# Kernel tuning notes

Measured on AMD Instinct MI355X. Metric: run time of the kernel, lower is better.

The kernel has to match this reference:

```python
import jax, jax.numpy as jnp
import numpy as np

B = 256          # graphs per batch
NC, NP = 16384, 131072   # compound / protein node counts
EC, EP = 131072, 2097152 # edge counts
D = 128


def _gconv(x, src, dst, W, b, n):
    # DGL GraphConv, norm='both': h = D_in^{-1/2} A D_out^{-1/2} x W + b
    ones = jnp.ones(src.shape, x.dtype)
    out_deg = jax.ops.segment_sum(ones, src, num_segments=n)
    in_deg = jax.ops.segment_sum(ones, dst, num_segments=n)
    ns = jax.lax.rsqrt(jnp.maximum(out_deg, 1.0))
    nd = jax.lax.rsqrt(jnp.maximum(in_deg, 1.0))
    h = (x * ns[:, None]) @ W           # apply weight before aggregation (same math, less traffic)
    m = jax.ops.segment_sum(h[src], dst, num_segments=n)  # SpMM aggregation
    return m * nd[:, None] + b


def _mean_nodes(x, gid, nb):
    s = jax.ops.segment_sum(x, gid, num_segments=nb)
    cnt = jax.ops.segment_sum(jnp.ones((x.shape[0],), x.dtype), gid, num_segments=nb)
    return s / jnp.maximum(cnt, 1.0)[:, None]


def setup_inputs() -> dict:
    key = jax.random.key(0)
    ks = jax.random.split(key, 24)
    s = 0.05
    inp = {
        "compound_feat": jax.random.normal(ks[0], (NC, 74), jnp.float32),
        "protein_feat": jax.random.normal(ks[1], (NP, 128), jnp.float32),
        # graph structure
        "c_src": jax.random.randint(ks[2], (EC,), 0, NC, jnp.int32),
        "c_dst": jax.random.randint(ks[3], (EC,), 0, NC, jnp.int32),
        "p_src": jax.random.randint(ks[4], (EP,), 0, NP, jnp.int32),
        "p_dst": jax.random.randint(ks[5], (EP,), 0, NP, jnp.int32),
        "c_gid": jax.random.randint(ks[6], (NC,), 0, B, jnp.int32),
        "p_gid": jax.random.randint(ks[7], (NP,), 0, B, jnp.int32),
        # GraphConv params
        "Wc1": jax.random.normal(ks[8], (74, D), jnp.float32) * s,
        "bc1": jnp.zeros((D,), jnp.float32),
        "Wc2": jax.random.normal(ks[9], (D, D), jnp.float32) * s,
        "bc2": jnp.zeros((D,), jnp.float32),
        "Wp1": jax.random.normal(ks[10], (128, D), jnp.float32) * s,
        "bp1": jnp.zeros((D,), jnp.float32),
        "Wp2": jax.random.normal(ks[11], (D, D), jnp.float32) * s,
        "bp2": jnp.zeros((D,), jnp.float32),
        # predictor MLP
        "Wf1": jax.random.normal(ks[12], (2 * D, D), jnp.float32) * s,
        "bf1": jnp.zeros((D,), jnp.float32),
        "Wf2": jax.random.normal(ks[13], (D, 1), jnp.float32) * s,
        "bf2": jnp.zeros((1,), jnp.float32),
    }
    return inp


def reference(compound_feat, protein_feat, c_src, c_dst, p_src, p_dst, c_gid, p_gid,
              Wc1, bc1, Wc2, bc2, Wp1, bp1, Wp2, bp2, Wf1, bf1, Wf2, bf2):
    c = jax.nn.relu(_gconv(compound_feat, c_src, c_dst, Wc1, bc1, NC))
    c = jax.nn.relu(_gconv(c, c_src, c_dst, Wc2, bc2, NC))
    c_global = _mean_nodes(c, c_gid, B)                     # [B, D]
    p = jax.nn.relu(_gconv(protein_feat, p_src, p_dst, Wp1, bp1, NP))
    p = jax.nn.relu(_gconv(p, p_src, p_dst, Wp2, bp2, NP))
    p_global = _mean_nodes(p, p_gid, B)                     # [B, D]
    combined = jnp.concatenate([c_global, p_global], axis=1)  # [B, 2D]
    h = jax.nn.relu(combined @ Wf1 + bf1)
    out = h @ Wf2 + bf2                                     # [B, 1]
    return out.squeeze(-1)
```

## Files before the change

kernel.cpp:

```cpp
#include <hip/hip_runtime.h>
#include <hip/hip_fp16.h>

#define D 128
#define SCH 4096
#define NBLK 256

typedef _Float16 half8 __attribute__((ext_vector_type(8)));
typedef float f32x4 __attribute__((ext_vector_type(4)));

struct HTask { const int* keys; int n; int shift; int* H; };
struct H6 { HTask t[6]; };

struct SPTask { const int* in; int n; int* part; };
struct SP6 { SPTask t[6]; };

struct SDTask { const int* in; int n; const int* part; int* out; int* total; };
struct SD6 { SDTask t[6]; };

struct ScTask { const int* k1; const int* k2; int n; int shift;
                const int* base1; const int* base2;
                int* o1; int* o2k; int* o2v; int mode; };
struct Sc4 { ScTask t[4]; };

struct CTask { const int* tmpk; const int* base; int n; int fine; int* deg; };
struct C4 { CTask t[4]; };

struct NTask { const int* outdeg; const int* indeg; float* ns; float* nd; int n; };
struct N2 { NTask t[2]; };

struct LTask { const int* tmpk; const int* tmpv; const int* base; int n;
               const int* rowptr; int shift; int fine; int* col; };
struct L2T { LTask t[2]; };

struct WPk { const float* W; _Float16* out; int K; };
struct W4 { WPk t[4]; };

struct GTask { const float* x; const float* ns; const _Float16* Wp; __half* h; int K; };
struct GemP { GTask t[2]; int nb0; };

struct ATask { const __half* h; const int* rowptr; const int* col;
               const float* nd; const float* b; void* out; int halfOut; };
struct AggP { ATask t[2]; int np; int ntot; };

struct MTask { const __half* x; const int* gbase; int n; const int* list; float* out; };
struct M2 { MTask t[2]; };


__global__ __launch_bounds__(256) void k_hist_all(H6 P) {
  HTask tk = P.t[blockIdx.y];
  __shared__ int bins[256];
  int blk = blockIdx.x, t = threadIdx.x;
  bins[t] = 0;
  __syncthreads();
  int per = (tk.n + NBLK - 1) / NBLK;
  int beg = blk * per, end = min(beg + per, tk.n);
  for (int i = beg + t; i < end; i += 256)
    atomicAdd(&bins[tk.keys[i] >> tk.shift], 1);
  __syncthreads();
  tk.H[t * NBLK + blk] = bins[t];
}

__global__ __launch_bounds__(256) void k_scan_part_all(SP6 P) {
  SPTask tk = P.t[blockIdx.y];
  int b = blockIdx.x, t = threadIdx.x;
  int base = b * SCH;
  int s = 0;
  for (int i = t; i < SCH; i += 256) {
    int idx = base + i;
    if (idx < tk.n) s += tk.in[idx];
  }
  __shared__ int red[256];
  red[t] = s;
  __syncthreads();
  for (int d = 128; d > 0; d >>= 1) {
    if (t < d) red[t] += red[t + d];
    __syncthreads();
  }
  if (t == 0) tk.part[b] = red[0];
}

__global__ __launch_bounds__(256) void k_scan_down_all(SD6 P) {
  SDTask tk = P.t[blockIdx.y];
  int b = blockIdx.x, t = threadIdx.x;
  int lane = t & 63, wid = t >> 6;
  __shared__ int wsum[4];
  if (b == 0 && t == 0 && tk.total) {
    int s = 0;
    for (int w = 0; w < (int)gridDim.x; ++w) s += tk.part[w];
    *tk.total = s;
  }
  int offset = 0;
  for (int w = 0; w < b; ++w) offset += tk.part[w];
  int base = b * SCH;
  if (base >= tk.n) return;
  int idx0 = base + t * 16;
  int v[16];
  int s = 0;
#pragma unroll
  for (int i = 0; i < 16; ++i) {
    int idx = idx0 + i;
    v[i] = (idx < tk.n) ? tk.in[idx] : 0;
    s += v[i];
  }
  int inc = s;
  for (int d = 1; d < 64; d <<= 1) {
    int u = __shfl_up(inc, d, 64);
    if (lane >= d) inc += u;
  }
  if (lane == 63) wsum[wid] = inc;
  __syncthreads();
  int woff = 0;
  for (int w = 0; w < wid; ++w) woff += wsum[w];
  int ex = offset + woff + inc - s;
#pragma unroll
  for (int i = 0; i < 16; ++i) {
    int idx = idx0 + i;
    if (idx < tk.n) tk.out[idx] = ex;
    ex += v[i];
  }
}

__global__ __launch_bounds__(256) void k_scatter_all(Sc4 P) {
  ScTask tk = P.t[blockIdx.y];
  __shared__ int curA[256], curB[256];
  int blk = blockIdx.x, t = threadIdx.x;
  curA[t] = tk.base1[t * NBLK + blk];
  if (tk.mode == 0) curB[t] = tk.base2[t * NBLK + blk];
  __syncthreads();
  int per = (tk.n + NBLK - 1) / NBLK;
  int beg = blk * per, end = min(beg + per, tk.n);
  if (tk.mode == 0) {
    for (int i = beg + t; i < end; i += 256) {
      int s = tk.k1[i], d = tk.k2[i];
      int pa = atomicAdd(&curA[s >> tk.shift], 1);
      tk.o1[pa] = s;
      int pb = atomicAdd(&curB[d >> tk.shift], 1);
      tk.o2k[pb] = d;
      tk.o2v[pb] = s;
    }
  } else {
    for (int i = beg + t; i < end; i += 256) {
      int pa = atomicAdd(&curA[tk.k1[i] >> tk.shift], 1);
      tk.o1[pa] = i;
    }
  }
}

__global__ __launch_bounds__(256) void k_l2count_all(C4 P) {
  CTask tk = P.t[blockIdx.y];
  __shared__ int bins[512];
  int b = blockIdx.x, t = threadIdx.x;
  for (int f = t; f < tk.fine; f += 256) bins[f] = 0;
  __syncthreads();
  int beg = tk.base[b * NBLK];
  int end = (b == NBLK - 1) ? tk.n : tk.base[(b + 1) * NBLK];
  for (int i = beg + t; i < end; i += 256)
    atomicAdd(&bins[tk.tmpk[i] & (tk.fine - 1)], 1);
  __syncthreads();
  for (int f = t; f < tk.fine; f += 256)
    tk.deg[b * tk.fine + f] = bins[f];
}

__global__ __launch_bounds__(256) void k_norms_all(N2 P) {
  NTask tk = P.t[blockIdx.y];
  int i = blockIdx.x * blockDim.x + threadIdx.x;
  if (i < tk.n) {
    tk.ns[i] = rsqrtf(fmaxf((float)tk.outdeg[i], 1.f));
    tk.nd[i] = rsqrtf(fmaxf((float)tk.indeg[i], 1.f));
  }
}

__global__ __launch_bounds__(256) void k_l2scatter_all(L2T P) {
  LTask tk = P.t[blockIdx.y];
  __shared__ int cur[512];
  int b = blockIdx.x, t = threadIdx.x;
  int v0 = b << tk.shift;
  for (int f = t; f < tk.fine; f += 256) cur[f] = tk.rowptr[v0 + f];
  __syncthreads();
  int beg = tk.base[b * NBLK];
  int end = (b == NBLK - 1) ? tk.n : tk.base[(b + 1) * NBLK];
  for (int i = beg + t; i < end; i += 256) {
    int pos = atomicAdd(&cur[tk.tmpk[i] & (tk.fine - 1)], 1);
    tk.col[pos] = tk.tmpv[i];
  }
}


__global__ __launch_bounds__(256) void k_wpack(W4 P) {
  WPk tk = P.t[blockIdx.y];
  int f = blockIdx.x;
  int kch = (tk.K + 31) >> 5;
  if (f >= (kch << 3)) return;
  int kc = f >> 3, nt = f & 7;
  int t = threadIdx.x;
  int l = t & 63, e0 = (t >> 6) << 1;
  int col = (nt << 4) + (l & 15);
  int kb = (kc << 5) + ((l >> 4) << 3);
#pragma unroll
  for (int e = e0; e < e0 + 2; ++e) {
    int k = kb + e;
    float v = (k < tk.K) ? tk.W[(size_t)k * D + col] : 0.f;
    tk.out[(((size_t)f * 64 + l) << 3) + e] = (_Float16)v;
  }
}

__global__ __launch_bounds__(256) void k_nl_gemm(GemP P) {
  __shared__ __align__(16) _Float16 Bs[32 * 64 * 8];
  int bx = blockIdx.x;
  GTask tk;
  int v0;
  if (bx < P.nb0) { tk = P.t[0]; v0 = bx * 128; }
  else            { tk = P.t[1]; v0 = (bx - P.nb0) * 128; }
  const int K = tk.K;
  const int kch = (K + 31) >> 5;
  int t = threadIdx.x, w = t >> 6, l = t & 63;

  {
    const uint4* src = (const uint4*)tk.Wp;
    uint4* dst = (uint4*)Bs;
    int n16 = kch << 9;
    for (int i = t; i < n16; i += 256) dst[i] = src[i];
  }
  __syncthreads();

  int row = l & 15;
  int ks = (l >> 4) << 3;
  int m0 = v0 + (w << 5);
  const float* x0 = tk.x + (size_t)(m0 + row) * K + ks;
  const float* x1 = tk.x + (size_t)(m0 + 16 + row) * K + ks;

  f32x4 acc[2][8];
  f32x4 zero = {0.f, 0.f, 0.f, 0.f};
#pragma unroll
  for (int i = 0; i < 2; ++i)
#pragma unroll
    for (int j = 0; j < 8; ++j) acc[i][j] = zero;

  for (int kc = 0; kc < kch; ++kc) {
    half8 a0, a1;
    if (K == D) {
      float4 p0 = *(const float4*)(x0 + (kc << 5));
      float4 p1 = *(const float4*)(x0 + (kc << 5) + 4);
      float4 q0 = *(const float4*)(x1 + (kc << 5));
      float4 q1 = *(const float4*)(x1 + (kc << 5) + 4);
      a0[0] = (_Float16)p0.x; a0[1] = (_Float16)p0.y;
      a0[2] = (_Float16)p0.z; a0[3] = (_Float16)p0.w;
      a0[4] = (_Float16)p1.x; a0[5] = (_Float16)p1.y;
      a0[6] = (_Float16)p1.z; a0[7] = (_Float16)p1.w;
      a1[0] = (_Float16)q0.x; a1[1] = (_Float16)q0.y;
      a1[2] = (_Float16)q0.z; a1[3] = (_Float16)q0.w;
      a1[4] = (_Float16)q1.x; a1[5] = (_Float16)q1.y;
      a1[6] = (_Float16)q1.z; a1[7] = (_Float16)q1.w;
    } else {
#pragma unroll
      for (int e = 0; e < 8; ++e) {
        int k = (kc << 5) + ks + e;
        a0[e] = (k < K) ? (_Float16)x0[(kc << 5) + e] : (_Float16)0.f;
        a1[e] = (k < K) ? (_Float16)x1[(kc << 5) + e] : (_Float16)0.f;
      }
    }
#pragma unroll
    for (int nt = 0; nt < 8; ++nt) {
      half8 b = *(const half8*)&Bs[(size_t)((((kc << 3) + nt) << 6) + l) << 3];
      acc[0][nt] = __builtin_amdgcn_mfma_f32_16x16x32_f16(a0, b, acc[0][nt], 0, 0, 0);
      acc[1][nt] = __builtin_amdgcn_mfma_f32_16x16x32_f16(a1, b, acc[1][nt], 0, 0, 0);
    }
  }

  int rr = (l >> 4) << 2;
  int c0 = l & 15;
#pragma unroll
  for (int mt = 0; mt < 2; ++mt) {
    int vb = m0 + (mt << 4) + rr;
    float s0 = tk.ns[vb], s1 = tk.ns[vb + 1];
    float s2 = tk.ns[vb + 2], s3 = tk.ns[vb + 3];
#pragma unroll
    for (int nt = 0; nt < 8; ++nt) {
      __half* hp = tk.h + (size_t)vb * D + (nt << 4) + c0;
      hp[0]     = __float2half_rn(acc[mt][nt][0] * s0);
      hp[D]     = __float2half_rn(acc[mt][nt][1] * s1);
      hp[2 * D] = __float2half_rn(acc[mt][nt][2] * s2);
      hp[3 * D] = __float2half_rn(acc[mt][nt][3] * s3);
    }
  }
}

__global__ __launch_bounds__(256) void k_aggregate(AggP P) {
  int wid = threadIdx.x >> 6;
  int lane = threadIdx.x & 63;
  int gv = blockIdx.x * 4 + wid;
  if (gv >= P.ntot) return;
  ATask tk;
  int v;
  if (gv < P.np) { tk = P.t[0]; v = gv; }
  else           { tk = P.t[1]; v = gv - P.np; }
  int beg = tk.rowptr[v], end = tk.rowptr[v + 1];
  int f0 = (lane & 15) * 8;
  int rsel = lane >> 4;
  const __half* h = tk.h;
  const int* col = tk.col;

  float acc[8];
#pragma unroll
  for (int k = 0; k < 8; ++k) acc[k] = 0.f;

  for (int j = beg; j < end; j += 8) {
    int j0 = j + rsel, j1 = j + 4 + rsel;
    if (j0 < end) {
      int c0 = col[j0];
      uint4 r = *(const uint4*)&h[(size_t)c0 * D + f0];
      const __half2* q = (const __half2*)&r;
#pragma unroll
      for (int k = 0; k < 4; ++k) {
        float2 f = __half22float2(q[k]);
        acc[2 * k] += f.x; acc[2 * k + 1] += f.y;
      }
    }
    if (j1 < end) {
      int c1 = col[j1];
      uint4 r = *(const uint4*)&h[(size_t)c1 * D + f0];
      const __half2* q = (const __half2*)&r;
#pragma unroll
      for (int k = 0; k < 4; ++k) {
        float2 f = __half22float2(q[k]);
        acc[2 * k] += f.x; acc[2 * k + 1] += f.y;
      }
    }
  }

#pragma unroll
  for (int k = 0; k < 8; ++k) {
    acc[k] += __shfl_down(acc[k], 32, 64);
    acc[k] += __shfl_down(acc[k], 16, 64);
  }

  if (rsel == 0) {
    float s = tk.nd[v];
    float4 b0 = *(const float4*)&tk.b[f0];
    float4 b1 = *(const float4*)&tk.b[f0 + 4];
    float r[8];
    r[0] = fmaxf(fmaf(acc[0], s, b0.x), 0.f);
    r[1] = fmaxf(fmaf(acc[1], s, b0.y), 0.f);
    r[2] = fmaxf(fmaf(acc[2], s, b0.z), 0.f);
    r[3] = fmaxf(fmaf(acc[3], s, b0.w), 0.f);
    r[4] = fmaxf(fmaf(acc[4], s, b1.x), 0.f);
    r[5] = fmaxf(fmaf(acc[5], s, b1.y), 0.f);
    r[6] = fmaxf(fmaf(acc[6], s, b1.z), 0.f);
    r[7] = fmaxf(fmaf(acc[7], s, b1.w), 0.f);
    if (tk.halfOut) {
      union { __half2 h2[4]; uint4 u; } pk;
#pragma unroll
      for (int k = 0; k < 4; ++k) {
        pk.h2[k].x = __float2half_rn(r[2 * k]);
        pk.h2[k].y = __float2half_rn(r[2 * k + 1]);
      }
      *(uint4*)&((__half*)tk.out)[(size_t)v * D + f0] = pk.u;
    } else {
      float4 o0 = {r[0], r[1], r[2], r[3]};
      float4 o1 = {r[4], r[5], r[6], r[7]};
      *(float4*)&((float*)tk.out)[(size_t)v * D + f0] = o0;
      *(float4*)&((float*)tk.out)[(size_t)v * D + f0 + 4] = o1;
    }
  }
}

__device__ __forceinline__ void acc_half4(float4& a, const __half* p) {
  uint2 r = *(const uint2*)p;
  __half2 q0 = *(__half2*)&r.x;
  __half2 q1 = *(__half2*)&r.y;
  float2 f0 = __half22float2(q0);
  float2 f1 = __half22float2(q1);
  a.x += f0.x; a.y += f0.y; a.z += f1.x; a.w += f1.y;
}

__global__ __launch_bounds__(256) void k_seg_mean(M2 P) {
  MTask tk = P.t[blockIdx.y];
  int g = blockIdx.x, t = threadIdx.x;
  int slot = t >> 5;
  int c = (t & 31) * 4;
  int beg = tk.gbase[g * NBLK];
  int end = (g == (int)gridDim.x - 1) ? tk.n : tk.gbase[(g + 1) * NBLK];
  const __half* x = tk.x;
  const int* list = tk.list;

  float4 a0 = make_float4(0.f, 0.f, 0.f, 0.f);
  float4 a1 = make_float4(0.f, 0.f, 0.f, 0.f);
  int j = beg + slot;
  for (; j + 8 < end; j += 16) {
    int s0 = list[j], s1 = list[j + 8];
    acc_half4(a0, x + (size_t)s0 * D + c);
    acc_half4(a1, x + (size_t)s1 * D + c);
  }
  if (j < end)
    acc_half4(a0, x + (size_t)list[j] * D + c);
  a0.x += a1.x; a0.y += a1.y; a0.z += a1.z; a0.w += a1.w;

  a0.x += __shfl_down(a0.x, 32, 64);
  a0.y += __shfl_down(a0.y, 32, 64);
  a0.z += __shfl_down(a0.z, 32, 64);
  a0.w += __shfl_down(a0.w, 32, 64);

  __shared__ float sred[4][32 * 4];
  int wid = t >> 6, lane = t & 63;
  if (lane < 32) *(float4*)&sred[wid][lane * 4] = a0;
  __syncthreads();
  if (t < 32) {
    float4 s0 = *(const float4*)&sred[0][t * 4];
    float4 s1 = *(const float4*)&sred[1][t * 4];
    float4 s2 = *(const float4*)&sred[2][t * 4];
    float4 s3 = *(const float4*)&sred[3][t * 4];
    float inv = 1.f / fmaxf((float)(end - beg), 1.f);
    float4 r;
    r.x = (s0.x + s1.x + s2.x + s3.x) * inv;
    r.y = (s0.y + s1.y + s2.y + s3.y) * inv;
    r.z = (s0.z + s1.z + s2.z + s3.z) * inv;
    r.w = (s0.w + s1.w + s2.w + s3.w) * inv;
    *(float4*)&tk.out[(size_t)g * D + c] = r;
  }
}

__global__ void k_mlp(const float* __restrict__ cg, const float* __restrict__ pg,
                      const float* __restrict__ Wf1, const float* __restrict__ bf1,
                      const float* __restrict__ Wf2, const float* __restrict__ bf2,
                      float* __restrict__ out) {
  __shared__ float xs[256];
  __shared__ float red[128];
  int b = blockIdx.x, t = threadIdx.x;
  xs[t] = cg[b * D + t];
  xs[128 + t] = pg[b * D + t];
  __syncthreads();
  float acc = bf1[t];
  for (int k = 0; k < 256; ++k) acc = fmaf(xs[k], Wf1[k * D + t], acc);
  float hv = fmaxf(acc, 0.f);
  red[t] = hv * Wf2[t];
  for (int d = 64; d > 0; d >>= 1) {
    __syncthreads();
    if (t < d) red[t] += red[t + d];
  }
  if (t == 0) out[b] = red[0] + bf2[0];
}


extern "C" void kernel_launch(void* const* d_in, const int* in_sizes, int n_in,
                              void* d_out, int out_size, void* d_ws, size_t ws_size,
                              hipStream_t stream) {
  const float* compound_feat = (const float*)d_in[0];
  const float* protein_feat  = (const float*)d_in[1];
  const int* c_src = (const int*)d_in[2];
  const int* c_dst = (const int*)d_in[3];
  const int* p_src = (const int*)d_in[4];
  const int* p_dst = (const int*)d_in[5];
  const int* c_gid = (const int*)d_in[6];
  const int* p_gid = (const int*)d_in[7];
  const float* Wc1 = (const float*)d_in[8];  const float* bc1 = (const float*)d_in[9];
  const float* Wc2 = (const float*)d_in[10]; const float* bc2 = (const float*)d_in[11];
  const float* Wp1 = (const float*)d_in[12]; const float* bp1 = (const float*)d_in[13];
  const float* Wp2 = (const float*)d_in[14]; const float* bp2 = (const float*)d_in[15];
  const float* Wf1 = (const float*)d_in[16]; const float* bf1 = (const float*)d_in[17];
  const float* Wf2 = (const float*)d_in[18]; const float* bf2 = (const float*)d_in[19];
  float* out = (float*)d_out;

  const int EC = in_sizes[2], EP = in_sizes[4];
  const int NC = in_sizes[6], NP = in_sizes[7];
  const int B  = out_size;
  const int KC = in_sizes[0] / NC;
  const int cshift = __builtin_ctz(NC / 256), cfine = NC / 256;
  const int pshift = __builtin_ctz(NP / 256), pfine = NP / 256;
  const int HN = 256 * NBLK;

  char* ws = (char*)d_ws;
  size_t off = 0;
  auto alloc = [&](size_t bytes) -> void* {
    void* p = ws + off;
    off += (bytes + 255) & ~(size_t)255;
    return p;
  };

  int* H0 = (int*)alloc((size_t)HN * 4);
  int* H1 = (int*)alloc((size_t)HN * 4);
  int* H2 = (int*)alloc((size_t)HN * 4);
  int* H3 = (int*)alloc((size_t)HN * 4);
  int* H4 = (int*)alloc((size_t)HN * 4);
  int* H5 = (int*)alloc((size_t)HN * 4);
  int* partH = (int*)alloc((size_t)6 * 32 * 4);
  int* partD = (int*)alloc((size_t)2 * 32 * 4);
  int* tmps_c = (int*)alloc((size_t)EC * 4);
  int* tmpd_c = (int*)alloc((size_t)EC * 4);
  int* tmpv_c = (int*)alloc((size_t)EC * 4);
  int* tmps_p = (int*)alloc((size_t)EP * 4);
  int* tmpd_p = (int*)alloc((size_t)EP * 4);
  int* tmpv_p = (int*)alloc((size_t)EP * 4);
  int* c_outdeg = (int*)alloc((size_t)NC * 4);
  int* c_indeg  = (int*)alloc((size_t)NC * 4);
  int* p_outdeg = (int*)alloc((size_t)NP * 4);
  int* p_indeg  = (int*)alloc((size_t)NP * 4);
  float* c_ns = (float*)alloc((size_t)NC * 4);
  float* c_nd = (float*)alloc((size_t)NC * 4);
  float* p_ns = (float*)alloc((size_t)NP * 4);
  float* p_nd = (float*)alloc((size_t)NP * 4);
  int* c_rowptr = (int*)alloc((size_t)(NC + 1) * 4);
  int* p_rowptr = (int*)alloc((size_t)(NP + 1) * 4);
  int* c_col   = (int*)alloc((size_t)EC * 4);
  int* p_col   = (int*)alloc((size_t)EP * 4);
  int* cg_list = (int*)alloc((size_t)NC * 4);
  int* pg_list = (int*)alloc((size_t)NP * 4);
  __half* c_h  = (__half*)alloc((size_t)NC * D * 2);
  float*  c_m1 = (float*) alloc((size_t)NC * D * 4);
  __half* c_m2 = (__half*)alloc((size_t)NC * D * 2);
  __half* p_h  = (__half*)alloc((size_t)NP * D * 2);
  float*  p_m1 = (float*) alloc((size_t)NP * D * 4);
  __half* p_m2 = (__half*)alloc((size_t)NP * D * 2);
  float* cg = (float*)alloc((size_t)B * D * 4);
  float* pg = (float*)alloc((size_t)B * D * 4);
  _Float16* wp_p1 = (_Float16*)alloc((size_t)32 * 1024);
  _Float16* wp_c1 = (_Float16*)alloc((size_t)32 * 1024);
  _Float16* wp_p2 = (_Float16*)alloc((size_t)32 * 1024);
  _Float16* wp_c2 = (_Float16*)alloc((size_t)32 * 1024);
  (void)ws_size; (void)n_in;

  {
    W4 PW = {{{Wp1, wp_p1, D}, {Wc1, wp_c1, KC}, {Wp2, wp_p2, D}, {Wc2, wp_c2, D}}};
    k_wpack<<<dim3(32, 4), 256, 0, stream>>>(PW);
  }
  {
    H6 P = {{{c_src, EC, cshift, H0}, {c_dst, EC, cshift, H1}, {c_gid, NC, 0, H2},
             {p_src, EP, pshift, H3}, {p_dst, EP, pshift, H4}, {p_gid, NP, 0, H5}}};
    k_hist_all<<<dim3(NBLK, 6), 256, 0, stream>>>(P);
  }
  {
    SP6 Pp = {{{H0, HN, partH + 0}, {H1, HN, partH + 32}, {H2, HN, partH + 64},
               {H3, HN, partH + 96}, {H4, HN, partH + 128}, {H5, HN, partH + 160}}};
    k_scan_part_all<<<dim3(16, 6), 256, 0, stream>>>(Pp);
    SD6 Pd = {{{H0, HN, partH + 0, H0, nullptr}, {H1, HN, partH + 32, H1, nullptr},
               {H2, HN, partH + 64, H2, nullptr}, {H3, HN, partH + 96, H3, nullptr},
               {H4, HN, partH + 128, H4, nullptr}, {H5, HN, partH + 160, H5, nullptr}}};
    k_scan_down_all<<<dim3(16, 6), 256, 0, stream>>>(Pd);
  }
  {
    Sc4 P = {{{c_src, c_dst, EC, cshift, H0, H1, tmps_c, tmpd_c, tmpv_c, 0},
              {p_src, p_dst, EP, pshift, H3, H4, tmps_p, tmpd_p, tmpv_p, 0},
              {c_gid, nullptr, NC, 0, H2, nullptr, cg_list, nullptr, nullptr, 1},
              {p_gid, nullptr, NP, 0, H5, nullptr, pg_list, nullptr, nullptr, 1}}};
    k_scatter_all<<<dim3(NBLK, 4), 256, 0, stream>>>(P);
  }
  {
    C4 P = {{{tmps_c, H0, EC, cfine, c_outdeg}, {tmpd_c, H1, EC, cfine, c_indeg},
             {tmps_p, H3, EP, pfine, p_outdeg}, {tmpd_p, H4, EP, pfine, p_indeg}}};
    k_l2count_all<<<dim3(NBLK, 4), 256, 0, stream>>>(P);
  }
  {
    SP6 Pp; Pp.t[0] = {c_indeg, NC, partD + 0}; Pp.t[1] = {p_indeg, NP, partD + 32};
    Pp.t[2] = Pp.t[3] = Pp.t[4] = Pp.t[5] = SPTask{c_indeg, 0, partD + 0};
    k_scan_part_all<<<dim3(32, 2), 256, 0, stream>>>(Pp);
    SD6 Pd; Pd.t[0] = {c_indeg, NC, partD + 0, c_rowptr, c_rowptr + NC};
    Pd.t[1] = {p_indeg, NP, partD + 32, p_rowptr, p_rowptr + NP};
    Pd.t[2] = Pd.t[3] = Pd.t[4] = Pd.t[5] = Pd.t[0];
    k_scan_down_all<<<dim3(32, 2), 256, 0, stream>>>(Pd);
  }
  {
    N2 P = {{{c_outdeg, c_indeg, c_ns, c_nd, NC}, {p_outdeg, p_indeg, p_ns, p_nd, NP}}};
    k_norms_all<<<dim3((NP + 255) / 256, 2), 256, 0, stream>>>(P);
  }
  {
    L2T P = {{{tmpd_c, tmpv_c, H1, EC, c_rowptr, cshift, cfine, c_col},
              {tmpd_p, tmpv_p, H4, EP, p_rowptr, pshift, pfine, p_col}}};
    k_l2scatter_all<<<dim3(NBLK, 2), 256, 0, stream>>>(P);
  }

  const int gnb = NP / 128 + NC / 128;
  const int anb = (NP + NC + 3) / 4;
  {
    GemP P = {{{protein_feat, p_ns, wp_p1, p_h, D}, {compound_feat, c_ns, wp_c1, c_h, KC}}, NP / 128};
    k_nl_gemm<<<gnb, 256, 0, stream>>>(P);
  }
  {
    AggP P = {{{p_h, p_rowptr, p_col, p_nd, bp1, p_m1, 0},
               {c_h, c_rowptr, c_col, c_nd, bc1, c_m1, 0}}, NP, NP + NC};
    k_aggregate<<<anb, 256, 0, stream>>>(P);
  }
  {
    GemP P = {{{p_m1, p_ns, wp_p2, p_h, D}, {c_m1, c_ns, wp_c2, c_h, D}}, NP / 128};
    k_nl_gemm<<<gnb, 256, 0, stream>>>(P);
  }
  {
    AggP P = {{{p_h, p_rowptr, p_col, p_nd, bp2, p_m2, 1},
               {c_h, c_rowptr, c_col, c_nd, bc2, c_m2, 1}}, NP, NP + NC};
    k_aggregate<<<anb, 256, 0, stream>>>(P);
  }
  {
    M2 P = {{{c_m2, H2, NC, cg_list, cg}, {p_m2, H5, NP, pg_list, pg}}};
    k_seg_mean<<<dim3(B, 2), 256, 0, stream>>>(P);
  }

  k_mlp<<<B, D, 0, stream>>>(cg, pg, Wf1, bf1, Wf2, bf2, out);
}
```

Baseline: 554.8 us.

## Drop src-side sort, count degrees atomically, store layer-1 output in fp16, deepen gather ILP

Removes the radix histogram, scatter and fine-count passes for source keys. Out- and in-degrees are now computed with global atomics over the raw edge arrays, which also eliminates the l2count kernel. The layer-1 aggregate output is stored as fp16 instead of fp32, and the second GEMM reads half8 directly, halving that intermediate traffic. The aggregation loop now issues four column loads before the gathers to increase memory-level parallelism. Global atomics on 2M edges may contend, and fp16 intermediates reduce precision.

```diff
diff --git a/kernel.cpp b/kernel.cpp
--- a/kernel.cpp
+++ b/kernel.cpp
@@ -17,13 +17,12 @@
 struct SDTask { const int* in; int n; const int* part; int* out; int* total; };
 struct SD6 { SDTask t[6]; };
 
+struct DgT { const int* keys; int n; int* deg; };
+struct Dg4 { DgT t[4]; };
+
 struct ScTask { const int* k1; const int* k2; int n; int shift;
-                const int* base1; const int* base2;
-                int* o1; int* o2k; int* o2v; int mode; };
+                const int* base; int* o1; int* o2; int mode; };
 struct Sc4 { ScTask t[4]; };
-
-struct CTask { const int* tmpk; const int* base; int n; int fine; int* deg; };
-struct C4 { CTask t[4]; };
 
 struct NTask { const int* outdeg; const int* indeg; float* ns; float* nd; int n; };
 struct N2 { NTask t[2]; };
@@ -35,7 +34,8 @@
 struct WPk { const float* W; _Float16* out; int K; };
 struct W4 { WPk t[4]; };
 
-struct GTask { const float* x; const float* ns; const _Float16* Wp; __half* h; int K; };
+struct GTask { const void* x; const float* ns; const _Float16* Wp; __half* h;
+               int K; int xh; };
 struct GemP { GTask t[2]; int nb0; };
 
 struct ATask { const __half* h; const int* rowptr; const int* col;
@@ -58,6 +58,13 @@
     atomicAdd(&bins[tk.keys[i] >> tk.shift], 1);
   __syncthreads();
   tk.H[t * NBLK + blk] = bins[t];
+}
+
+__global__ __launch_bounds__(256) void k_deg_all(Dg4 P) {
+  DgT tk = P.t[blockIdx.y];
+  int stride = gridDim.x * 256;
+  for (int i = blockIdx.x * 256 + threadIdx.x; i < tk.n; i += stride)
+    atomicAdd(&tk.deg[tk.keys[i]], 1);
 }
 
 __global__ __launch_bounds__(256) void k_scan_part_all(SP6 P) {
@@ -122,43 +129,25 @@
 
 __global__ __launch_bounds__(256) void k_scatter_all(Sc4 P) {
   ScTask tk = P.t[blockIdx.y];
-  __shared__ int curA[256], curB[256];
+  __shared__ int cur[256];
   int blk = blockIdx.x, t = threadIdx.x;
-  curA[t] = tk.base1[t * NBLK + blk];
-  if (tk.mode == 0) curB[t] = tk.base2[t * NBLK + blk];
+  cur[t] = tk.base[t * NBLK + blk];
   __syncthreads();
   int per = (tk.n + NBLK - 1) / NBLK;
   int beg = blk * per, end = min(beg + per, tk.n);
   if (tk.mode == 0) {
     for (int i = beg + t; i < end; i += 256) {
-      int s = tk.k1[i], d = tk.k2[i];
-      int pa = atomicAdd(&curA[s >> tk.shift], 1);
-      tk.o1[pa] = s;
-      int pb = atomicAdd(&curB[d >> tk.shift], 1);
-      tk.o2k[pb] = d;
-      tk.o2v[pb] = s;
+      int d = tk.k1[i], s = tk.k2[i];
+      int p = atomicAdd(&cur[d >> tk.shift], 1);
+      tk.o1[p] = d;
+      tk.o2[p] = s;
     }
   } else {
     for (int i = beg + t; i < end; i += 256) {
-      int pa = atomicAdd(&curA[tk.k1[i] >> tk.shift], 1);
-      tk.o1[pa] = i;
-    }
-  }
-}
-
-__global__ __launch_bounds__(256) void k_l2count_all(C4 P) {
-  CTask tk = P.t[blockIdx.y];
-  __shared__ int bins[512];
-  int b = blockIdx.x, t = threadIdx.x;
-  for (int f = t; f < tk.fine; f += 256) bins[f] = 0;
-  __syncthreads();
-  int beg = tk.base[b * NBLK];
-  int end = (b == NBLK - 1) ? tk.n : tk.base[(b + 1) * NBLK];
-  for (int i = beg + t; i < end; i += 256)
-    atomicAdd(&bins[tk.tmpk[i] & (tk.fine - 1)], 1);
-  __syncthreads();
-  for (int f = t; f < tk.fine; f += 256)
-    tk.deg[b * tk.fine + f] = bins[f];
+      int p = atomicAdd(&cur[tk.k1[i] >> tk.shift], 1);
+      tk.o1[p] = i;
+    }
+  }
 }
 
 __global__ __launch_bounds__(256) void k_norms_all(N2 P) {
@@ -226,8 +215,15 @@
   int row = l & 15;
   int ks = (l >> 4) << 3;
   int m0 = v0 + (w << 5);
-  const float* x0 = tk.x + (size_t)(m0 + row) * K + ks;
-  const float* x1 = tk.x + (size_t)(m0 + 16 + row) * K + ks;
+  const float* xf0 = nullptr; const float* xf1 = nullptr;
+  const _Float16* xh0 = nullptr; const _Float16* xh1 = nullptr;
+  if (tk.xh) {
+    xh0 = (const _Float16*)tk.x + (size_t)(m0 + row) * D + ks;
+    xh1 = xh0 + (size_t)16 * D;
+  } else {
+    xf0 = (const float*)tk.x + (size_t)(m0 + row) * K + ks;
+    xf1 = xf0 + (size_t)16 * K;
+  }
 
   f32x4 acc[2][8];
   f32x4 zero = {0.f, 0.f, 0.f, 0.f};
@@ -238,11 +234,14 @@
 
   for (int kc = 0; kc < kch; ++kc) {
     half8 a0, a1;
-    if (K == D) {
-      float4 p0 = *(const float4*)(x0 + (kc << 5));
-      float4 p1 = *(const float4*)(x0 + (kc << 5) + 4);
-      float4 q0 = *(const float4*)(x1 + (kc << 5));
-      float4 q1 = *(const float4*)(x1 + (kc << 5) + 4);
+    if (tk.xh) {
+      a0 = *(const half8*)(xh0 + (kc << 5));
+      a1 = *(const half8*)(xh1 + (kc << 5));
+    } else if (K == D) {
+      float4 p0 = *(const float4*)(xf0 + (kc << 5));
+      float4 p1 = *(const float4*)(xf0 + (kc << 5) + 4);
+      float4 q0 = *(const float4*)(xf1 + (kc << 5));
+      float4 q1 = *(const float4*)(xf1 + (kc << 5) + 4);
       a0[0] = (_Float16)p0.x; a0[1] = (_Float16)p0.y;
       a0[2] = (_Float16)p0.z; a0[3] = (_Float16)p0.w;
       a0[4] = (_Float16)p1.x; a0[5] = (_Float16)p1.y;
@@ -255,8 +254,8 @@
 #pragma unroll
       for (int e = 0; e < 8; ++e) {
         int k = (kc << 5) + ks + e;
-        a0[e] = (k < K) ? (_Float16)x0[(kc << 5) + e] : (_Float16)0.f;
-        a1[e] = (k < K) ? (_Float16)x1[(kc << 5) + e] : (_Float16)0.f;
+        a0[e] = (k < K) ? (_Float16)xf0[(kc << 5) + e] : (_Float16)0.f;
+        a1[e] = (k < K) ? (_Float16)xf1[(kc << 5) + e] : (_Float16)0.f;
       }
     }
 #pragma unroll
@@ -304,26 +303,24 @@
 #pragma unroll
   for (int k = 0; k < 8; ++k) acc[k] = 0.f;
 
-  for (int j = beg; j < end; j += 8) {
-    int j0 = j + rsel, j1 = j + 4 + rsel;
-    if (j0 < end) {
-      int c0 = col[j0];
-      uint4 r = *(const uint4*)&h[(size_t)c0 * D + f0];
-      const __half2* q = (const __half2*)&r;
-#pragma unroll
-      for (int k = 0; k < 4; ++k) {
-        float2 f = __half22float2(q[k]);
-        acc[2 * k] += f.x; acc[2 * k + 1] += f.y;
-      }
-    }
-    if (j1 < end) {
-      int c1 = col[j1];
-      uint4 r = *(const uint4*)&h[(size_t)c1 * D + f0];
-      const __half2* q = (const __half2*)&r;
-#pragma unroll
-      for (int k = 0; k < 4; ++k) {
-        float2 f = __half22float2(q[k]);
-        acc[2 * k] += f.x; acc[2 * k + 1] += f.y;
+  for (int j = beg; j < end; j += 16) {
+    int jj[4];
+    int cc[4];
+#pragma unroll
+    for (int q = 0; q < 4; ++q) {
+      jj[q] = j + 4 * q + rsel;
+      cc[q] = (jj[q] < end) ? col[jj[q]] : -1;
+    }
+#pragma unroll
+    for (int q = 0; q < 4; ++q) {
+      if (cc[q] >= 0) {
+        uint4 r = *(const uint4*)&h[(size_t)cc[q] * D + f0];
+        const __half2* p = (const __half2*)&r;
+#pragma unroll
+        for (int k = 0; k < 4; ++k) {
+          float2 f = __half22float2(p[k]);
+          acc[2 * k] += f.x; acc[2 * k + 1] += f.y;
+        }
       }
     }
   }
@@ -476,24 +473,21 @@
     return p;
   };
 
-  int* H0 = (int*)alloc((size_t)HN * 4);
   int* H1 = (int*)alloc((size_t)HN * 4);
   int* H2 = (int*)alloc((size_t)HN * 4);
-  int* H3 = (int*)alloc((size_t)HN * 4);
   int* H4 = (int*)alloc((size_t)HN * 4);
   int* H5 = (int*)alloc((size_t)HN * 4);
   int* partH = (int*)alloc((size_t)6 * 32 * 4);
   int* partD = (int*)alloc((size_t)2 * 32 * 4);
-  int* tmps_c = (int*)alloc((size_t)EC * 4);
   int* tmpd_c = (int*)alloc((size_t)EC * 4);
   int* tmpv_c = (int*)alloc((size_t)EC * 4);
-  int* tmps_p = (int*)alloc((size_t)EP * 4);
   int* tmpd_p = (int*)alloc((size_t)EP * 4);
   int* tmpv_p = (int*)alloc((size_t)EP * 4);
-  int* c_outdeg = (int*)alloc((size_t)NC * 4);
-  int* c_indeg  = (int*)alloc((size_t)NC * 4);
-  int* p_outdeg = (int*)alloc((size_t)NP * 4);
-  int* p_indeg  = (int*)alloc((size_t)NP * 4);
+  int* degs = (int*)alloc(((size_t)NC * 2 + (size_t)NP * 2) * 4);
+  int* c_outdeg = degs;
+  int* c_indeg  = degs + NC;
+  int* p_outdeg = degs + 2 * NC;
+  int* p_indeg  = degs + 2 * NC + NP;
   float* c_ns = (float*)alloc((size_t)NC * 4);
   float* c_nd = (float*)alloc((size_t)NC * 4);
   float* p_ns = (float*)alloc((size_t)NP * 4);
@@ -505,10 +499,10 @@
   int* cg_list = (int*)alloc((size_t)NC * 4);
   int* pg_list = (int*)alloc((size_t)NP * 4);
   __half* c_h  = (__half*)alloc((size_t)NC * D * 2);
-  float*  c_m1 = (float*) alloc((size_t)NC * D * 4);
+  __half* c_m1 = (__half*)alloc((size_t)NC * D * 2);
   __half* c_m2 = (__half*)alloc((size_t)NC * D * 2);
   __half* p_h  = (__half*)alloc((size_t)NP * D * 2);
-  float*  p_m1 = (float*) alloc((size_t)NP * D * 4);
+  __half* p_m1 = (__half*)alloc((size_t)NP * D * 2);
   __half* p_m2 = (__half*)alloc((size_t)NP * D * 2);
   float* cg = (float*)alloc((size_t)B * D * 4);
   float* pg = (float*)alloc((size_t)B * D * 4);
@@ -518,35 +512,40 @@
   _Float16* wp_c2 = (_Float16*)alloc((size_t)32 * 1024);
   (void)ws_size; (void)n_in;
 
+  hipMemsetAsync(degs, 0, ((size_t)NC * 2 + (size_t)NP * 2) * 4, stream);
   {
     W4 PW = {{{Wp1, wp_p1, D}, {Wc1, wp_c1, KC}, {Wp2, wp_p2, D}, {Wc2, wp_c2, D}}};
     k_wpack<<<dim3(32, 4), 256, 0, stream>>>(PW);
   }
   {
-    H6 P = {{{c_src, EC, cshift, H0}, {c_dst, EC, cshift, H1}, {c_gid, NC, 0, H2},
-             {p_src, EP, pshift, H3}, {p_dst, EP, pshift, H4}, {p_gid, NP, 0, H5}}};
-    k_hist_all<<<dim3(NBLK, 6), 256, 0, stream>>>(P);
-  }
-  {
-    SP6 Pp = {{{H0, HN, partH + 0}, {H1, HN, partH + 32}, {H2, HN, partH + 64},
-               {H3, HN, partH + 96}, {H4, HN, partH + 128}, {H5, HN, partH + 160}}};
-    k_scan_part_all<<<dim3(16, 6), 256, 0, stream>>>(Pp);
-    SD6 Pd = {{{H0, HN, partH + 0, H0, nullptr}, {H1, HN, partH + 32, H1, nullptr},
-               {H2, HN, partH + 64, H2, nullptr}, {H3, HN, partH + 96, H3, nullptr},
-               {H4, HN, partH + 128, H4, nullptr}, {H5, HN, partH + 160, H5, nullptr}}};
-    k_scan_down_all<<<dim3(16, 6), 256, 0, stream>>>(Pd);
-  }
-  {
-    Sc4 P = {{{c_src, c_dst, EC, cshift, H0, H1, tmps_c, tmpd_c, tmpv_c, 0},
-              {p_src, p_dst, EP, pshift, H3, H4, tmps_p, tmpd_p, tmpv_p, 0},
-              {c_gid, nullptr, NC, 0, H2, nullptr, cg_list, nullptr, nullptr, 1},
-              {p_gid, nullptr, NP, 0, H5, nullptr, pg_list, nullptr, nullptr, 1}}};
+    H6 P; P.t[0] = {c_dst, EC, cshift, H1}; P.t[1] = {c_gid, NC, 0, H2};
+    P.t[2] = {p_dst, EP, pshift, H4}; P.t[3] = {p_gid, NP, 0, H5};
+    P.t[4] = P.t[5] = P.t[0];
+    k_hist_all<<<dim3(NBLK, 4), 256, 0, stream>>>(P);
+  }
+  {
+    Dg4 P = {{{c_src, EC, c_outdeg}, {c_dst, EC, c_indeg},
+              {p_src, EP, p_outdeg}, {p_dst, EP, p_indeg}}};
+    k_deg_all<<<dim3(2048, 4), 256, 0, stream>>>(P);
+  }
+  {
+    SP6 Pp; Pp.t[0] = {H1, HN, partH + 0}; Pp.t[1] = {H2, HN, partH + 32};
+    Pp.t[2] = {H4, HN, partH + 64}; Pp.t[3] = {H5, HN, partH + 96};
+    Pp.t[4] = Pp.t[5] = Pp.t[0];
+    k_scan_part_all<<<dim3(16, 4), 256, 0, stream>>>(Pp);
+    SD6 Pd; Pd.t[0] = {H1, HN, partH + 0, H1, nullptr};
+    Pd.t[1] = {H2, HN, partH + 32, H2, nullptr};
+    Pd.t[2] = {H4, HN, partH + 64, H4, nullptr};
+    Pd.t[3] = {H5, HN, partH + 96, H5, nullptr};
+    Pd.t[4] = Pd.t[5] = Pd.t[0];
+    k_scan_down_all<<<dim3(16, 4), 256, 0, stream>>>(Pd);
+  }
+  {
+    Sc4 P = {{{c_dst, c_src, EC, cshift, H1, tmpd_c, tmpv_c, 0},
+              {p_dst, p_src, EP, pshift, H4, tmpd_p, tmpv_p, 0},
+              {c_gid, nullptr, NC, 0, H2, cg_list, nullptr, 1},
+              {p_gid, nullptr, NP, 0, H5, pg_list, nullptr, 1}}};
     k_scatter_all<<<dim3(NBLK, 4), 256, 0, stream>>>(P);
-  }
-  {
-    C4 P = {{{tmps_c, H0, EC, cfine, c_outdeg}, {tmpd_c, H1, EC, cfine, c_indeg},
-             {tmps_p, H3, EP, pfine, p_outdeg}, {tmpd_p, H4, EP, pfine, p_indeg}}};
-    k_l2count_all<<<dim3(NBLK, 4), 256, 0, stream>>>(P);
   }
   {
     SP6 Pp; Pp.t[0] = {c_indeg, NC, partD + 0}; Pp.t[1] = {p_indeg, NP, partD + 32};
@@ -570,16 +569,17 @@
   const int gnb = NP / 128 + NC / 128;
   const int anb = (NP + NC + 3) / 4;
   {
-    GemP P = {{{protein_feat, p_ns, wp_p1, p_h, D}, {compound_feat, c_ns, wp_c1, c_h, KC}}, NP / 128};
+    GemP P = {{{protein_feat, p_ns, wp_p1, p_h, D, 0},
+               {compound_feat, c_ns, wp_c1, c_h, KC, 0}}, NP / 128};
     k_nl_gemm<<<gnb, 256, 0, stream>>>(P);
   }
   {
-    AggP P = {{{p_h, p_rowptr, p_col, p_nd, bp1, p_m1, 0},
-               {c_h, c_rowptr, c_col, c_nd, bc1, c_m1, 0}}, NP, NP + NC};
+    AggP P = {{{p_h, p_rowptr, p_col, p_nd, bp1, p_m1, 1},
+               {c_h, c_rowptr, c_col, c_nd, bc1, c_m1, 1}}, NP, NP + NC};
     k_aggregate<<<anb, 256, 0, stream>>>(P);
   }
   {
-    GemP P = {{{p_m1, p_ns, wp_p2, p_h, D}, {c_m1, c_ns, wp_c2, c_h, D}}, NP / 128};
+    GemP P = {{{p_m1, p_ns, wp_p2, p_h, D, 1}, {c_m1, c_ns, wp_c2, c_h, D, 1}}, NP / 128};
     k_nl_gemm<<<gnb, 256, 0, stream>>>(P);
   }
   {
```

New measurement: 668.3 us. 20.5% more time.
